# Optimization experiments

Measured on AMD Instinct MI355X. Metric: run time of the kernel, lower is better.

Reference implementation:

```python
import jax, jax.numpy as jnp
import numpy as np

D_MODEL = 512
N_HEADS = 8
D_K = D_MODEL // N_HEADS
D_FF = 2048
EPS = 1e-5  # torch LayerNorm default


def _layer_norm(x, g, b):
    mu = jnp.mean(x, axis=-1, keepdims=True)
    var = jnp.mean(jnp.square(x - mu), axis=-1, keepdims=True)
    return (x - mu) * jax.lax.rsqrt(var + EPS) * g + b


def setup_inputs() -> dict:
    key = jax.random.key(0)
    ks = jax.random.split(key, 16)
    s_in = 1.0 / np.sqrt(D_MODEL)
    s_ff = 1.0 / np.sqrt(D_FF)
    # Linear weights stored as [in, out] (transpose of torch convention)
    return {
        "x": jax.random.normal(ks[0], (2, 2048, D_MODEL), jnp.float32),
        "wq_w": jax.random.uniform(ks[1], (D_MODEL, D_MODEL), jnp.float32, -s_in, s_in),
        "wq_b": jax.random.uniform(ks[2], (D_MODEL,), jnp.float32, -s_in, s_in),
        "wk_w": jax.random.uniform(ks[3], (D_MODEL, D_MODEL), jnp.float32, -s_in, s_in),
        "wk_b": jax.random.uniform(ks[4], (D_MODEL,), jnp.float32, -s_in, s_in),
        "wv_w": jax.random.uniform(ks[5], (D_MODEL, D_MODEL), jnp.float32, -s_in, s_in),
        "wv_b": jax.random.uniform(ks[6], (D_MODEL,), jnp.float32, -s_in, s_in),
        "wo_w": jax.random.uniform(ks[7], (D_MODEL, D_MODEL), jnp.float32, -s_in, s_in),
        "wo_b": jax.random.uniform(ks[8], (D_MODEL,), jnp.float32, -s_in, s_in),
        "ln1_g": jnp.ones((D_MODEL,), jnp.float32),
        "ln1_b": jnp.zeros((D_MODEL,), jnp.float32),
        "fc1_w": jax.random.uniform(ks[9], (D_MODEL, D_FF), jnp.float32, -s_in, s_in),
        "fc1_b": jax.random.uniform(ks[10], (D_FF,), jnp.float32, -s_in, s_in),
        "fc2_w": jax.random.uniform(ks[11], (D_FF, D_MODEL), jnp.float32, -s_ff, s_ff),
        "fc2_b": jax.random.uniform(ks[12], (D_MODEL,), jnp.float32, -s_ff, s_ff),
        "ln2_g": jnp.ones((D_MODEL,), jnp.float32),
        "ln2_b": jnp.zeros((D_MODEL,), jnp.float32),
    }


def reference(x, wq_w, wq_b, wk_w, wk_b, wv_w, wv_b, wo_w, wo_b,
              ln1_g, ln1_b, fc1_w, fc1_b, fc2_w, fc2_b, ln2_g, ln2_b):
    B, T, _ = x.shape
    # --- multi-head self-attention (mask=None; dropout in eval mode = identity) ---
    q = (x @ wq_w + wq_b).reshape(B, T, N_HEADS, D_K).transpose(0, 2, 1, 3)  # [B,H,T,d_k]
    k = (x @ wk_w + wk_b).reshape(B, T, N_HEADS, D_K).transpose(0, 2, 1, 3)
    v = (x @ wv_w + wv_b).reshape(B, T, N_HEADS, D_K).transpose(0, 2, 1, 3)
    scores = jnp.einsum("bhqd,bhkd->bhqk", q, k) / np.sqrt(D_K).astype(np.float32)
    attn = jax.nn.softmax(scores, axis=-1)  # [B,H,T,T]
    ctx = jnp.einsum("bhqk,bhkd->bhqd", attn, v)
    ctx = ctx.transpose(0, 2, 1, 3).reshape(B, T, D_MODEL)
    attn_out = ctx @ wo_w + wo_b
    # --- residual + LN1 ---
    h = _layer_norm(x + attn_out, ln1_g, ln1_b)
    # --- FFN (relu) + residual + LN2 ---
    ffn = jax.nn.relu(h @ fc1_w + fc1_b) @ fc2_w + fc2_b
    out = _layer_norm(h + ffn, ln2_g, ln2_b)
    return out, attn
```

## Files before the change

### kernel.cpp

```cpp
#include <hip/hip_runtime.h>
#include <hip/hip_bf16.h>

typedef __hip_bfloat16 bf16;
typedef __attribute__((ext_vector_type(8))) short short8v;
typedef __attribute__((ext_vector_type(4))) float f32x4;

#define B_   2
#define T_   2048
#define D_   512
#define H_   8
#define DK_  64
#define DFF_ 2048
#define M_   (B_*T_)

static __device__ __forceinline__ float b2f(bf16 v) { return __bfloat162float(v); }
static __device__ __forceinline__ bf16  f2b(float v){ return __float2bfloat16(v); }

static __device__ __forceinline__ float ldin(const void* p, size_t i, bool bf) {
    return bf ? __bfloat162float(((const bf16*)p)[i]) : ((const float*)p)[i];
}
static __device__ __forceinline__ void stout(void* p, size_t i, float v, bool bf) {
    if (bf) ((bf16*)p)[i] = __float2bfloat16(v);
    else    ((float*)p)[i] = v;
}
static __device__ __forceinline__ short hi_of(float v) {
    bf16 h = f2b(v);
    return *(const short*)&h;
}
static __device__ __forceinline__ short lo_of(float v) {
    bf16 h = f2b(v);
    bf16 l = f2b(v - b2f(h));
    return *(const short*)&l;
}

__global__ void detect_dtype(const unsigned int* __restrict__ x, int* __restrict__ flag)
{
    __shared__ int cnt;
    if (threadIdx.x == 0) cnt = 0;
    __syncthreads();
    int local = 0;
    for (int i = threadIdx.x; i < 1024; i += 256) {
        unsigned int lo = x[i] & 0xFFFFu;
        float v = __uint_as_float(lo << 16);
        float a = fabsf(v);
        if (a > 1e-3f && a < 16.f) local++;
    }
    atomicAdd(&cnt, local);
    __syncthreads();
    if (threadIdx.x == 0) *flag = (cnt > 512) ? 1 : 0;
}

__global__ __launch_bounds__(256)
void split_x(const void* __restrict__ X, bf16* __restrict__ xh,
             bf16* __restrict__ xl, const int* __restrict__ flag)
{
    const bool bf = (*flag != 0);
    const size_t i = ((size_t)blockIdx.x * 256 + threadIdx.x) * 8;
    if (bf) {
        *(short8v*)(xh + i) = *(const short8v*)((const bf16*)X + i);
    } else {
        const float* Xf = (const float*)X + i;
        const float4 f0 = *(const float4*)(Xf);
        const float4 f1 = *(const float4*)(Xf + 4);
        const float vals[8] = {f0.x, f0.y, f0.z, f0.w, f1.x, f1.y, f1.z, f1.w};
        short8v hi, lo;
        #pragma unroll
        for (int j = 0; j < 8; ++j) {
            short th = hi_of(vals[j]);
            short tl = lo_of(vals[j]);
            hi[j] = th;
            lo[j] = tl;
        }
        *(short8v*)(xh + i) = hi;
        *(short8v*)(xl + i) = lo;
    }
}

__global__ __launch_bounds__(256)
void transpose_w(const void* __restrict__ W, bf16* __restrict__ oh,
                 bf16* __restrict__ ol, const int* __restrict__ flag,
                 int K, int N, float scale)
{
    const bool bf = (*flag != 0);
    __shared__ float tile[32][33];
    const int n0 = blockIdx.x * 32;
    const int k0 = blockIdx.y * 32;
    const int c  = threadIdx.x & 31;
    const int r8 = threadIdx.x >> 5;

    #pragma unroll
    for (int i = 0; i < 4; ++i) {
        int r = r8 + i * 8;
        tile[r][c] = ldin(W, (size_t)(k0 + r) * N + n0 + c, bf) * scale;
    }
    __syncthreads();
    #pragma unroll
    for (int i = 0; i < 4; ++i) {
        int r = r8 + i * 8;
        float v = tile[c][r];
        bf16 h = f2b(v);
        oh[(size_t)(n0 + r) * K + k0 + c] = h;
        if (!bf) ol[(size_t)(n0 + r) * K + k0 + c] = f2b(v - b2f(h));
    }
}

template<int BN, int NA, int RELU, int OBF>
__global__ __launch_bounds__(256)
void gemm_mfma(const bf16* __restrict__ Ahg, const bf16* __restrict__ Alg,
               const bf16* __restrict__ BTh, const bf16* __restrict__ BTl,
               const void* __restrict__ bias, const int* __restrict__ flag,
               void* __restrict__ C, bf16* __restrict__ Cl,
               int M, int N, int K, float bscale)
{
    constexpr int BM = 128;
    constexpr int FM = 4;
    constexpr int FN = BN / 32;
    const bool bfw   = (*flag != 0);
    const bool useAl = !(NA == 1 && bfw);
    const bool useBl = !bfw;

    __shared__ short As[2][BM][40];
    __shared__ short Bs[2][BN][40];

    const int tid  = threadIdx.x;
    const int lane = tid & 63;
    const int wave = tid >> 6;
    const int wm   = wave >> 1;
    const int wn   = wave & 1;
    const int rowBase = blockIdx.y * BM;
    const int colBase = blockIdx.x * BN;

    const int fr = lane & 15;
    const int kb = (lane >> 4) * 8;

    const int arow = tid >> 1;
    const int acol = (tid & 1) * 16;
    const int brow = (BN == 128) ? (tid >> 1) : (tid >> 2);
    const int bcol = (BN == 128) ? ((tid & 1) * 16) : ((tid & 3) * 8);

    const bf16* aHs = Ahg + (size_t)(rowBase + arow) * K + acol;
    const bf16* aLs = Alg + (size_t)(rowBase + arow) * K + acol;
    const bf16* bHs = BTh + (size_t)(colBase + brow) * K + bcol;
    const bf16* bLs = BTl + (size_t)(colBase + brow) * K + bcol;

    f32x4 acc[FM][FN] = {};

    for (int k0 = 0; k0 < K; k0 += 32) {
        __syncthreads();
        *(short8v*)&As[0][arow][acol]     = *(const short8v*)(aHs + k0);
        *(short8v*)&As[0][arow][acol + 8] = *(const short8v*)(aHs + k0 + 8);
        if (useAl) {
            *(short8v*)&As[1][arow][acol]     = *(const short8v*)(aLs + k0);
            *(short8v*)&As[1][arow][acol + 8] = *(const short8v*)(aLs + k0 + 8);
        }
        if (BN == 128) {
            *(short8v*)&Bs[0][brow][bcol]     = *(const short8v*)(bHs + k0);
            *(short8v*)&Bs[0][brow][bcol + 8] = *(const short8v*)(bHs + k0 + 8);
            if (useBl) {
                *(short8v*)&Bs[1][brow][bcol]     = *(const short8v*)(bLs + k0);
                *(short8v*)&Bs[1][brow][bcol + 8] = *(const short8v*)(bLs + k0 + 8);
            }
        } else {
            *(short8v*)&Bs[0][brow][bcol] = *(const short8v*)(bHs + k0);
            if (useBl)
                *(short8v*)&Bs[1][brow][bcol] = *(const short8v*)(bLs + k0);
        }
        __syncthreads();

        short8v aH[FM], aL[FM], bH[FN], bL[FN];
        #pragma unroll
        for (int f = 0; f < FM; ++f)
            aH[f] = *(const short8v*)&As[0][wm * 64 + f * 16 + fr][kb];
        if (useAl) {
            #pragma unroll
            for (int f = 0; f < FM; ++f)
                aL[f] = *(const short8v*)&As[1][wm * 64 + f * 16 + fr][kb];
        }
        #pragma unroll
        for (int f = 0; f < FN; ++f)
            bH[f] = *(const short8v*)&Bs[0][wn * (BN/2) + f * 16 + fr][kb];
        if (useBl) {
            #pragma unroll
            for (int f = 0; f < FN; ++f)
                bL[f] = *(const short8v*)&Bs[1][wn * (BN/2) + f * 16 + fr][kb];
        }

        #pragma unroll
        for (int i = 0; i < FM; ++i)
            #pragma unroll
            for (int j = 0; j < FN; ++j) {
                acc[i][j] = __builtin_amdgcn_mfma_f32_16x16x32_bf16(aH[i], bH[j], acc[i][j], 0, 0, 0);
                if (useAl)
                    acc[i][j] = __builtin_amdgcn_mfma_f32_16x16x32_bf16(aL[i], bH[j], acc[i][j], 0, 0, 0);
                if (useBl)
                    acc[i][j] = __builtin_amdgcn_mfma_f32_16x16x32_bf16(aH[i], bL[j], acc[i][j], 0, 0, 0);
            }
    }

    const int rq = (lane >> 4) * 4;
    #pragma unroll
    for (int j = 0; j < FN; ++j) {
        const int col = colBase + wn * (BN/2) + j * 16 + fr;
        const float bv = ldin(bias, col, bfw) * bscale;
        #pragma unroll
        for (int i = 0; i < FM; ++i) {
            #pragma unroll
            for (int q = 0; q < 4; ++q) {
                float v = acc[i][j][q] + bv;
                if (RELU) v = fmaxf(v, 0.f);
                const int row = rowBase + wm * 64 + i * 16 + rq + q;
                if (OBF == 0) {
                    ((float*)C)[(size_t)row * N + col] = v;
                } else if (OBF == 1) {
                    ((bf16*)C)[(size_t)row * N + col] = f2b(v);
                } else if (OBF == 2) {
                    size_t idx = (size_t)row * N + col;
                    bf16 h = f2b(v);
                    ((bf16*)C)[idx] = h;
                    Cl[idx] = f2b(v - b2f(h));
                } else {
                    ((bf16*)C)[(size_t)col * M + row] = f2b(v);
                }
            }
        }
    }
}

__global__ __launch_bounds__(256)
void attn_mfma(const bf16* __restrict__ Qb, const bf16* __restrict__ Kb,
               const bf16* __restrict__ VTb, void* __restrict__ dout,
               const int* __restrict__ flag,
               bf16* __restrict__ ctxh, bf16* __restrict__ ctxl)
{
    const bool bf = (*flag != 0);
    const int tid  = threadIdx.x;
    const int lane = tid & 63;
    const int wave = tid >> 6;
    const int wm = wave >> 1, wn = wave & 1;
    const int q0 = blockIdx.x * 64;
    const int h  = blockIdx.y;
    const int b  = blockIdx.z;
    const size_t OFFOUT = (size_t)M_ * D_;

    __shared__ short Qs[64][72];
    __shared__ short Ks[64][72];
    __shared__ short Vs[64][72];
    __shared__ short Ps[64][72];
    __shared__ float Lp[2][64];
    __shared__ float invl_s[64];

    const int fr = lane & 15;
    const int kb = (lane >> 4) * 8;

    #pragma unroll
    for (int l = 0; l < 2; ++l) {
        int idx = tid + l * 256;
        int r = idx >> 3, c8 = (idx & 7) * 8;
        *(short8v*)&Qs[r][c8] =
            *(const short8v*)(Qb + (size_t)(b*T_ + q0 + r) * D_ + h*DK_ + c8);
    }

    float lsum[2][4] = {};

    for (int kt = 0; kt < T_/64; ++kt) {
        __syncthreads();
        #pragma unroll
        for (int l = 0; l < 2; ++l) {
            int idx = tid + l * 256;
            int r = idx >> 3, c8 = (idx & 7) * 8;
            *(short8v*)&Ks[r][c8] =
                *(const short8v*)(Kb + (size_t)(b*T_ + kt*64 + r) * D_ + h*DK_ + c8);
        }
        __syncthreads();

        short8v aF[2][2], bF[2][2];
        #pragma unroll
        for (int i = 0; i < 2; ++i)
            #pragma unroll
            for (int k2 = 0; k2 < 2; ++k2)
                aF[i][k2] = *(const short8v*)&Qs[wm*32 + i*16 + fr][kb + k2*32];
        #pragma unroll
        for (int j = 0; j < 2; ++j)
            #pragma unroll
            for (int k2 = 0; k2 < 2; ++k2)
                bF[j][k2] = *(const short8v*)&Ks[wn*32 + j*16 + fr][kb + k2*32];

        #pragma unroll
        for (int i = 0; i < 2; ++i)
            #pragma unroll
            for (int j = 0; j < 2; ++j) {
                f32x4 s = {};
                s = __builtin_amdgcn_mfma_f32_16x16x32_bf16(aF[i][0], bF[j][0], s, 0, 0, 0);
                s = __builtin_amdgcn_mfma_f32_16x16x32_bf16(aF[i][1], bF[j][1], s, 0, 0, 0);
                #pragma unroll
                for (int q = 0; q < 4; ++q)
                    lsum[i][q] += __expf(fminf(s[q], 60.f));
            }
    }

    #pragma unroll
    for (int i = 0; i < 2; ++i)
        #pragma unroll
        for (int q = 0; q < 4; ++q) {
            float v = lsum[i][q];
            #pragma unroll
            for (int o = 8; o; o >>= 1) v += __shfl_xor(v, o, 16);
            lsum[i][q] = v;
        }
    if (fr == 0) {
        #pragma unroll
        for (int i = 0; i < 2; ++i)
            #pragma unroll
            for (int q = 0; q < 4; ++q)
                Lp[wn][wm*32 + i*16 + (lane>>4)*4 + q] = lsum[i][q];
    }
    __syncthreads();
    if (tid < 64) invl_s[tid] = 1.f / (Lp[0][tid] + Lp[1][tid]);
    __syncthreads();

    float il[2][4];
    #pragma unroll
    for (int i = 0; i < 2; ++i)
        #pragma unroll
        for (int q = 0; q < 4; ++q)
            il[i][q] = invl_s[wm*32 + i*16 + (lane>>4)*4 + q];

    f32x4 cacc[2][2] = {};

    for (int kt = 0; kt < T_/64; ++kt) {
        __syncthreads();
        #pragma unroll
        for (int l = 0; l < 2; ++l) {
            int idx = tid + l * 256;
            int r = idx >> 3, c8 = (idx & 7) * 8;
            *(short8v*)&Ks[r][c8] =
                *(const short8v*)(Kb + (size_t)(b*T_ + kt*64 + r) * D_ + h*DK_ + c8);
            *(short8v*)&Vs[r][c8] =
                *(const short8v*)(VTb + (size_t)(h*DK_ + r) * M_ + b*T_ + kt*64 + c8);
        }
        __syncthreads();

        short8v aF[2][2], bF[2][2];
        #pragma unroll
        for (int i = 0; i < 2; ++i)
            #pragma unroll
            for (int k2 = 0; k2 < 2; ++k2)
                aF[i][k2] = *(const short8v*)&Qs[wm*32 + i*16 + fr][kb + k2*32];
        #pragma unroll
        for (int j = 0; j < 2; ++j)
            #pragma unroll
            for (int k2 = 0; k2 < 2; ++k2)
                bF[j][k2] = *(const short8v*)&Ks[wn*32 + j*16 + fr][kb + k2*32];

        f32x4 sacc[2][2];
        #pragma unroll
        for (int i = 0; i < 2; ++i)
            #pragma unroll
            for (int j = 0; j < 2; ++j) {
                f32x4 s = {};
                s = __builtin_amdgcn_mfma_f32_16x16x32_bf16(aF[i][0], bF[j][0], s, 0, 0, 0);
                s = __builtin_amdgcn_mfma_f32_16x16x32_bf16(aF[i][1], bF[j][1], s, 0, 0, 0);
                sacc[i][j] = s;
            }

        #pragma unroll
        for (int i = 0; i < 2; ++i)
            #pragma unroll
            for (int j = 0; j < 2; ++j) {
                #pragma unroll
                for (int q = 0; q < 4; ++q) {
                    const int qq = wm*32 + i*16 + (lane>>4)*4 + q;
                    const int kk = wn*32 + j*16 + fr;
                    float p = __expf(fminf(sacc[i][j][q], 60.f)) * il[i][q];
                    bf16 pb = f2b(p);
                    Ps[qq][kk] = *(const short*)&pb;
                    size_t go = OFFOUT + ((size_t)((b*H_+h)*T_ + q0 + qq))*T_ + kt*64 + kk;
                    if (bf) ((bf16*)dout)[go] = pb;
                    else    ((float*)dout)[go] = p;
                }
            }
        __syncthreads();

        short8v pF[2][2], vF[2][2];
        #pragma unroll
        for (int i = 0; i < 2; ++i)
            #pragma unroll
            for (int k2 = 0; k2 < 2; ++k2)
                pF[i][k2] = *(const short8v*)&Ps[wm*32 + i*16 + fr][kb + k2*32];
        #pragma unroll
        for (int j = 0; j < 2; ++j)
            #pragma unroll
            for (int k2 = 0; k2 < 2; ++k2)
                vF[j][k2] = *(const short8v*)&Vs[wn*32 + j*16 + fr][kb + k2*32];

        #pragma unroll
        for (int i = 0; i < 2; ++i)
            #pragma unroll
            for (int j = 0; j < 2; ++j) {
                cacc[i][j] = __builtin_amdgcn_mfma_f32_16x16x32_bf16(pF[i][0], vF[j][0], cacc[i][j], 0, 0, 0);
                cacc[i][j] = __builtin_amdgcn_mfma_f32_16x16x32_bf16(pF[i][1], vF[j][1], cacc[i][j], 0, 0, 0);
            }
    }

    #pragma unroll
    for (int i = 0; i < 2; ++i)
        #pragma unroll
        for (int j = 0; j < 2; ++j)
            #pragma unroll
            for (int q = 0; q < 4; ++q) {
                const int qq = wm*32 + i*16 + (lane>>4)*4 + q;
                size_t idx = (size_t)(b*T_ + q0 + qq)*D_ + h*DK_ + wn*32 + j*16 + fr;
                float v = cacc[i][j][q];
                bf16 hh = f2b(v);
                ctxh[idx] = hh;
                ctxl[idx] = f2b(v - b2f(hh));
            }
}

__global__ __launch_bounds__(256)
void ln1_kernel(const void* X, const float* __restrict__ A,
                const void* g, const void* be,
                const int* __restrict__ flag, float* __restrict__ out,
                bf16* __restrict__ hh, bf16* __restrict__ hl)
{
    const bool bf = (*flag != 0);
    const int row = blockIdx.x;
    const int tid = threadIdx.x;
    const size_t base = (size_t)row * D_;

    float v0 = ldin(X, base + tid, bf)       + A[base + tid];
    float v1 = ldin(X, base + 256 + tid, bf) + A[base + 256 + tid];
    float s  = v0 + v1;
    float sq = v0*v0 + v1*v1;
    #pragma unroll
    for (int o = 32; o; o >>= 1) { s += __shfl_xor(s, o, 64); sq += __shfl_xor(sq, o, 64); }

    __shared__ float rs[4], rq[4];
    if ((tid & 63) == 0) { rs[tid >> 6] = s; rq[tid >> 6] = sq; }
    __syncthreads();
    s  = rs[0] + rs[1] + rs[2] + rs[3];
    sq = rq[0] + rq[1] + rq[2] + rq[3];

    float mu   = s * (1.f / D_);
    float var  = sq * (1.f / D_) - mu * mu;
    float rstd = rsqrtf(var + 1e-5f);
    float y0 = (v0 - mu) * rstd * ldin(g, tid, bf)       + ldin(be, tid, bf);
    float y1 = (v1 - mu) * rstd * ldin(g, 256 + tid, bf) + ldin(be, 256 + tid, bf);
    out[base + tid]       = y0;
    out[base + 256 + tid] = y1;
    bf16 h0 = f2b(y0); hh[base + tid] = h0;       hl[base + tid]       = f2b(y0 - b2f(h0));
    bf16 h1 = f2b(y1); hh[base + 256 + tid] = h1; hl[base + 256 + tid] = f2b(y1 - b2f(h1));
}

__global__ __launch_bounds__(256)
void ln2_kernel(const float* __restrict__ Hf, const float* __restrict__ F,
                const void* g, const void* be,
                const int* __restrict__ flag, void* out)
{
    const bool bf = (*flag != 0);
    const int row = blockIdx.x;
    const int tid = threadIdx.x;
    const size_t base = (size_t)row * D_;

    float v0 = Hf[base + tid]       + F[base + tid];
    float v1 = Hf[base + 256 + tid] + F[base + 256 + tid];
    float s  = v0 + v1;
    float sq = v0*v0 + v1*v1;
    #pragma unroll
    for (int o = 32; o; o >>= 1) { s += __shfl_xor(s, o, 64); sq += __shfl_xor(sq, o, 64); }

    __shared__ float rs[4], rq[4];
    if ((tid & 63) == 0) { rs[tid >> 6] = s; rq[tid >> 6] = sq; }
    __syncthreads();
    s  = rs[0] + rs[1] + rs[2] + rs[3];
    sq = rq[0] + rq[1] + rq[2] + rq[3];

    float mu   = s * (1.f / D_);
    float var  = sq * (1.f / D_) - mu * mu;
    float rstd = rsqrtf(var + 1e-5f);
    stout(out, base + tid,       (v0 - mu) * rstd * ldin(g, tid, bf)       + ldin(be, tid, bf),       bf);
    stout(out, base + 256 + tid, (v1 - mu) * rstd * ldin(g, 256 + tid, bf) + ldin(be, 256 + tid, bf), bf);
}

extern "C" void kernel_launch(void* const* d_in, const int* in_sizes, int n_in,
                              void* d_out, int out_size, void* d_ws, size_t ws_size,
                              hipStream_t stream)
{
    const void* x     = d_in[0];
    const void* wq_w  = d_in[1];
    const void* wq_b  = d_in[2];
    const void* wk_w  = d_in[3];
    const void* wk_b  = d_in[4];
    const void* wv_w  = d_in[5];
    const void* wv_b  = d_in[6];
    const void* wo_w  = d_in[7];
    const void* wo_b  = d_in[8];
    const void* ln1_g = d_in[9];
    const void* ln1_b = d_in[10];
    const void* fc1_w = d_in[11];
    const void* fc1_b = d_in[12];
    const void* fc2_w = d_in[13];
    const void* fc2_b = d_in[14];
    const void* ln2_g = d_in[15];
    const void* ln2_b = d_in[16];

    char* W = (char*)d_ws;
    const size_t MB = 1u << 20;
    bf16*  xh    = (bf16*)(W + 0*MB);
    bf16*  xl    = (bf16*)(W + 4*MB);
    bf16*  Qb    = (bf16*)(W + 8*MB);
    bf16*  Kb    = (bf16*)(W + 12*MB);
    bf16*  VTb   = (bf16*)(W + 16*MB);
    bf16*  ctxh  = (bf16*)(W + 20*MB);
    bf16*  ctxl  = (bf16*)(W + 24*MB);
    bf16*  ffn1h = (bf16*)(W + 0*MB);
    bf16*  ffn1l = (bf16*)(W + 16*MB);
    float* ao    = (float*)(W + 32*MB);
    float* ffn2  = (float*)(W + 32*MB);
    float* h     = (float*)(W + 40*MB);
    bf16*  hh    = (bf16*)(W + 48*MB);
    bf16*  hl    = (bf16*)(W + 52*MB);
    bf16*  tw    = (bf16*)(W + 56*MB);
    const size_t SW = (size_t)D_ * D_;
    const size_t SF = (size_t)D_ * DFF_;
    bf16* wqTh = tw;                 bf16* wqTl = wqTh + SW;
    bf16* wkTh = wqTl + SW;          bf16* wkTl = wkTh + SW;
    bf16* wvTh = wkTl + SW;          bf16* wvTl = wvTh + SW;
    bf16* woTh = wvTl + SW;          bf16* woTl = woTh + SW;
    bf16* f1Th = woTl + SW;          bf16* f1Tl = f1Th + SF;
    bf16* f2Th = f1Tl + SF;          bf16* f2Tl = f2Th + SF;
    int*  flag = (int*)(f2Tl + SF);

    dim3 blk(256);

    detect_dtype<<<1, 256, 0, stream>>>((const unsigned int*)x, flag);

    transpose_w<<<dim3(D_/32,   D_/32),   blk, 0, stream>>>(wq_w,  wqTh, wqTl, flag, D_,   D_,   0.125f);
    transpose_w<<<dim3(D_/32,   D_/32),   blk, 0, stream>>>(wk_w,  wkTh, wkTl, flag, D_,   D_,   1.f);
    transpose_w<<<dim3(D_/32,   D_/32),   blk, 0, stream>>>(wv_w,  wvTh, wvTl, flag, D_,   D_,   1.f);
    transpose_w<<<dim3(D_/32,   D_/32),   blk, 0, stream>>>(wo_w,  woTh, woTl, flag, D_,   D_,   1.f);
    transpose_w<<<dim3(DFF_/32, D_/32),   blk, 0, stream>>>(fc1_w, f1Th, f1Tl, flag, D_,   DFF_, 1.f);
    transpose_w<<<dim3(D_/32,   DFF_/32), blk, 0, stream>>>(fc2_w, f2Th, f2Tl, flag, DFF_, D_,   1.f);

    split_x<<<(M_*D_)/(256*8), blk, 0, stream>>>(x, xh, xl, flag);

    gemm_mfma<64,1,0,1><<<dim3(D_/64,  M_/128), blk, 0, stream>>>(xh, xl, wqTh, wqTl, wq_b, flag, Qb,  nullptr, M_, D_, D_, 0.125f);
    gemm_mfma<64,1,0,1><<<dim3(D_/64,  M_/128), blk, 0, stream>>>(xh, xl, wkTh, wkTl, wk_b, flag, Kb,  nullptr, M_, D_, D_, 1.f);
    gemm_mfma<64,1,0,3><<<dim3(D_/64,  M_/128), blk, 0, stream>>>(xh, xl, wvTh, wvTl, wv_b, flag, VTb, nullptr, M_, D_, D_, 1.f);

    attn_mfma<<<dim3(T_/64, H_, B_), blk, 0, stream>>>(Qb, Kb, VTb, d_out, flag, ctxh, ctxl);

    gemm_mfma<64,0,0,0><<<dim3(D_/64,  M_/128), blk, 0, stream>>>(ctxh, ctxl, woTh, woTl, wo_b, flag, ao, nullptr, M_, D_, D_, 1.f);

    ln1_kernel<<<M_, 256, 0, stream>>>(x, ao, ln1_g, ln1_b, flag, h, hh, hl);

    gemm_mfma<128,0,1,2><<<dim3(DFF_/128, M_/128), blk, 0, stream>>>(hh, hl, f1Th, f1Tl, fc1_b, flag, ffn1h, ffn1l, M_, DFF_, D_, 1.f);
    gemm_mfma<64,0,0,0><<<dim3(D_/64,   M_/128), blk, 0, stream>>>(ffn1h, ffn1l, f2Th, f2Tl, fc2_b, flag, ffn2, nullptr, M_, D_, DFF_, 1.f);

    ln2_kernel<<<M_, 256, 0, stream>>>(h, ffn2, ln2_g, ln2_b, flag, d_out);
}
```

Measured before the change: 686.1 us.

## Fuse weight prep and QKV GEMMs, shrink GEMM tiles, drop fp32 LN1 output

The six weight-transpose launches become one prep_weights kernel, and the three Q/K/V projections become one gemm_qkv launch over a concatenated 1536-wide weight. Every GEMM moves from a 128-row tile to a 64x64 tile, which gives more blocks for the small matrices. LN1 no longer writes a separate fp32 copy of h; LN2 rebuilds it from the bf16 hi/lo split. The aims are less launch overhead, better occupancy, and less memory traffic, at the cost of less reuse per tile and a small precision change in the residual.

```diff
diff --git a/kernel.cpp b/kernel.cpp
--- a/kernel.cpp
+++ b/kernel.cpp
@@ -77,14 +77,30 @@
 }
 
 __global__ __launch_bounds__(256)
-void transpose_w(const void* __restrict__ W, bf16* __restrict__ oh,
-                 bf16* __restrict__ ol, const int* __restrict__ flag,
-                 int K, int N, float scale)
+void prep_weights(const void* __restrict__ wq, const void* __restrict__ wk,
+                  const void* __restrict__ wv, const void* __restrict__ wo,
+                  const void* __restrict__ f1, const void* __restrict__ f2,
+                  bf16* __restrict__ qkvTh, bf16* __restrict__ qkvTl,
+                  bf16* __restrict__ woTh,  bf16* __restrict__ woTl,
+                  bf16* __restrict__ f1Th,  bf16* __restrict__ f1Tl,
+                  bf16* __restrict__ f2Th,  bf16* __restrict__ f2Tl,
+                  const int* __restrict__ flag)
 {
     const bool bf = (*flag != 0);
+    int bid = blockIdx.x;
+    const void* W; bf16 *oh, *ol; int K, N; float scale = 1.f;
+    if (bid < 256)       { W = wq; oh = qkvTh;          ol = qkvTl;          K = 512;  N = 512;  scale = 0.125f; }
+    else if (bid < 512)  { W = wk; oh = qkvTh + 262144; ol = qkvTl + 262144; K = 512;  N = 512;  bid -= 256; }
+    else if (bid < 768)  { W = wv; oh = qkvTh + 524288; ol = qkvTl + 524288; K = 512;  N = 512;  bid -= 512; }
+    else if (bid < 1024) { W = wo; oh = woTh;           ol = woTl;           K = 512;  N = 512;  bid -= 768; }
+    else if (bid < 2048) { W = f1; oh = f1Th;           ol = f1Tl;           K = 512;  N = 2048; bid -= 1024; }
+    else                 { W = f2; oh = f2Th;           ol = f2Tl;           K = 2048; N = 512;  bid -= 2048; }
+
+    const int ntn = N / 32;
+    const int n0 = (bid % ntn) * 32;
+    const int k0 = (bid / ntn) * 32;
+
     __shared__ float tile[32][33];
-    const int n0 = blockIdx.x * 32;
-    const int k0 = blockIdx.y * 32;
     const int c  = threadIdx.x & 31;
     const int r8 = threadIdx.x >> 5;
 
@@ -104,94 +120,162 @@
     }
 }
 
-template<int BN, int NA, int RELU, int OBF>
+__global__ __launch_bounds__(256)
+void gemm_qkv(const bf16* __restrict__ Ahg, const bf16* __restrict__ Alg,
+              const bf16* __restrict__ BTh, const bf16* __restrict__ BTl,
+              const void* __restrict__ qbias, const void* __restrict__ kbias,
+              const void* __restrict__ vbias, const int* __restrict__ flag,
+              bf16* __restrict__ Qb, bf16* __restrict__ Kb, bf16* __restrict__ VTb)
+{
+    const int  K     = D_;
+    const bool bfw   = (*flag != 0);
+    const bool useAl = !bfw;
+    const bool useBl = !bfw;
+
+    __shared__ short As[2][64][40];
+    __shared__ short Bs[2][64][40];
+
+    const int tid  = threadIdx.x;
+    const int lane = tid & 63;
+    const int wave = tid >> 6;
+    const int wm   = wave >> 1;
+    const int wn   = wave & 1;
+    const int rowBase = blockIdx.y * 64;
+    const int colBase = blockIdx.x * 64;
+
+    const int fr = lane & 15;
+    const int kb = (lane >> 4) * 8;
+    const int srow = tid >> 2;
+    const int skc  = (tid & 3) * 8;
+
+    const bf16* aHs = Ahg + (size_t)(rowBase + srow) * K + skc;
+    const bf16* aLs = Alg + (size_t)(rowBase + srow) * K + skc;
+    const bf16* bHs = BTh + (size_t)(colBase + srow) * K + skc;
+    const bf16* bLs = BTl + (size_t)(colBase + srow) * K + skc;
+
+    f32x4 acc[2][2] = {};
+
+    for (int k0 = 0; k0 < K; k0 += 32) {
+        __syncthreads();
+        *(short8v*)&As[0][srow][skc] = *(const short8v*)(aHs + k0);
+        if (useAl) *(short8v*)&As[1][srow][skc] = *(const short8v*)(aLs + k0);
+        *(short8v*)&Bs[0][srow][skc] = *(const short8v*)(bHs + k0);
+        if (useBl) *(short8v*)&Bs[1][srow][skc] = *(const short8v*)(bLs + k0);
+        __syncthreads();
+
+        short8v aH[2], aL[2], bH[2], bL[2];
+        #pragma unroll
+        for (int f = 0; f < 2; ++f) {
+            aH[f] = *(const short8v*)&As[0][wm * 32 + f * 16 + fr][kb];
+            bH[f] = *(const short8v*)&Bs[0][wn * 32 + f * 16 + fr][kb];
+        }
+        if (useAl) {
+            #pragma unroll
+            for (int f = 0; f < 2; ++f)
+                aL[f] = *(const short8v*)&As[1][wm * 32 + f * 16 + fr][kb];
+        }
+        if (useBl) {
+            #pragma unroll
+            for (int f = 0; f < 2; ++f)
+                bL[f] = *(const short8v*)&Bs[1][wn * 32 + f * 16 + fr][kb];
+        }
+
+        #pragma unroll
+        for (int i = 0; i < 2; ++i)
+            #pragma unroll
+            for (int j = 0; j < 2; ++j) {
+                acc[i][j] = __builtin_amdgcn_mfma_f32_16x16x32_bf16(aH[i], bH[j], acc[i][j], 0, 0, 0);
+                if (useAl)
+                    acc[i][j] = __builtin_amdgcn_mfma_f32_16x16x32_bf16(aL[i], bH[j], acc[i][j], 0, 0, 0);
+                if (useBl)
+                    acc[i][j] = __builtin_amdgcn_mfma_f32_16x16x32_bf16(aH[i], bL[j], acc[i][j], 0, 0, 0);
+            }
+    }
+
+    const int region = colBase >> 9;
+    const void* bp = (region == 0) ? qbias : (region == 1) ? kbias : vbias;
+    const float bs = (region == 0) ? 0.125f : 1.f;
+    const int rq = (lane >> 4) * 4;
+    #pragma unroll
+    for (int j = 0; j < 2; ++j) {
+        const int col = colBase + wn * 32 + j * 16 + fr;
+        const int lc  = col - (region << 9);
+        const float bv = ldin(bp, lc, bfw) * bs;
+        #pragma unroll
+        for (int i = 0; i < 2; ++i) {
+            #pragma unroll
+            for (int q = 0; q < 4; ++q) {
+                float v = acc[i][j][q] + bv;
+                const int row = rowBase + wm * 32 + i * 16 + rq + q;
+                if (region == 0)      Qb[(size_t)row * D_ + lc] = f2b(v);
+                else if (region == 1) Kb[(size_t)row * D_ + lc] = f2b(v);
+                else                  VTb[(size_t)lc * M_ + row] = f2b(v);
+            }
+        }
+    }
+}
+
+template<int RELU, int OBF>
 __global__ __launch_bounds__(256)
 void gemm_mfma(const bf16* __restrict__ Ahg, const bf16* __restrict__ Alg,
                const bf16* __restrict__ BTh, const bf16* __restrict__ BTl,
                const void* __restrict__ bias, const int* __restrict__ flag,
                void* __restrict__ C, bf16* __restrict__ Cl,
-               int M, int N, int K, float bscale)
-{
-    constexpr int BM = 128;
-    constexpr int FM = 4;
-    constexpr int FN = BN / 32;
+               int M, int N, int K)
+{
     const bool bfw   = (*flag != 0);
-    const bool useAl = !(NA == 1 && bfw);
     const bool useBl = !bfw;
 
-    __shared__ short As[2][BM][40];
-    __shared__ short Bs[2][BN][40];
+    __shared__ short As[2][64][40];
+    __shared__ short Bs[2][64][40];
 
     const int tid  = threadIdx.x;
     const int lane = tid & 63;
     const int wave = tid >> 6;
     const int wm   = wave >> 1;
     const int wn   = wave & 1;
-    const int rowBase = blockIdx.y * BM;
-    const int colBase = blockIdx.x * BN;
+    const int rowBase = blockIdx.y * 64;
+    const int colBase = blockIdx.x * 64;
 
     const int fr = lane & 15;
     const int kb = (lane >> 4) * 8;
-
-    const int arow = tid >> 1;
-    const int acol = (tid & 1) * 16;
-    const int brow = (BN == 128) ? (tid >> 1) : (tid >> 2);
-    const int bcol = (BN == 128) ? ((tid & 1) * 16) : ((tid & 3) * 8);
-
-    const bf16* aHs = Ahg + (size_t)(rowBase + arow) * K + acol;
-    const bf16* aLs = Alg + (size_t)(rowBase + arow) * K + acol;
-    const bf16* bHs = BTh + (size_t)(colBase + brow) * K + bcol;
-    const bf16* bLs = BTl + (size_t)(colBase + brow) * K + bcol;
-
-    f32x4 acc[FM][FN] = {};
+    const int srow = tid >> 2;
+    const int skc  = (tid & 3) * 8;
+
+    const bf16* aHs = Ahg + (size_t)(rowBase + srow) * K + skc;
+    const bf16* aLs = Alg + (size_t)(rowBase + srow) * K + skc;
+    const bf16* bHs = BTh + (size_t)(colBase + srow) * K + skc;
+    const bf16* bLs = BTl + (size_t)(colBase + srow) * K + skc;
+
+    f32x4 acc[2][2] = {};
 
     for (int k0 = 0; k0 < K; k0 += 32) {
         __syncthreads();
-        *(short8v*)&As[0][arow][acol]     = *(const short8v*)(aHs + k0);
-        *(short8v*)&As[0][arow][acol + 8] = *(const short8v*)(aHs + k0 + 8);
-        if (useAl) {
-            *(short8v*)&As[1][arow][acol]     = *(const short8v*)(aLs + k0);
-            *(short8v*)&As[1][arow][acol + 8] = *(const short8v*)(aLs + k0 + 8);
-        }
-        if (BN == 128) {
-            *(short8v*)&Bs[0][brow][bcol]     = *(const short8v*)(bHs + k0);
-            *(short8v*)&Bs[0][brow][bcol + 8] = *(const short8v*)(bHs + k0 + 8);
-            if (useBl) {
-                *(short8v*)&Bs[1][brow][bcol]     = *(const short8v*)(bLs + k0);
-                *(short8v*)&Bs[1][brow][bcol + 8] = *(const short8v*)(bLs + k0 + 8);
-            }
-        } else {
-            *(short8v*)&Bs[0][brow][bcol] = *(const short8v*)(bHs + k0);
-            if (useBl)
-                *(short8v*)&Bs[1][brow][bcol] = *(const short8v*)(bLs + k0);
-        }
-        __syncthreads();
-
-        short8v aH[FM], aL[FM], bH[FN], bL[FN];
-        #pragma unroll
-        for (int f = 0; f < FM; ++f)
-            aH[f] = *(const short8v*)&As[0][wm * 64 + f * 16 + fr][kb];
-        if (useAl) {
-            #pragma unroll
-            for (int f = 0; f < FM; ++f)
-                aL[f] = *(const short8v*)&As[1][wm * 64 + f * 16 + fr][kb];
-        }
-        #pragma unroll
-        for (int f = 0; f < FN; ++f)
-            bH[f] = *(const short8v*)&Bs[0][wn * (BN/2) + f * 16 + fr][kb];
+        *(short8v*)&As[0][srow][skc] = *(const short8v*)(aHs + k0);
+        *(short8v*)&As[1][srow][skc] = *(const short8v*)(aLs + k0);
+        *(short8v*)&Bs[0][srow][skc] = *(const short8v*)(bHs + k0);
+        if (useBl) *(short8v*)&Bs[1][srow][skc] = *(const short8v*)(bLs + k0);
+        __syncthreads();
+
+        short8v aH[2], aL[2], bH[2], bL[2];
+        #pragma unroll
+        for (int f = 0; f < 2; ++f) {
+            aH[f] = *(const short8v*)&As[0][wm * 32 + f * 16 + fr][kb];
+            aL[f] = *(const short8v*)&As[1][wm * 32 + f * 16 + fr][kb];
+            bH[f] = *(const short8v*)&Bs[0][wn * 32 + f * 16 + fr][kb];
+        }
         if (useBl) {
             #pragma unroll
-            for (int f = 0; f < FN; ++f)
-                bL[f] = *(const short8v*)&Bs[1][wn * (BN/2) + f * 16 + fr][kb];
-        }
-
-        #pragma unroll
-        for (int i = 0; i < FM; ++i)
-            #pragma unroll
-            for (int j = 0; j < FN; ++j) {
+            for (int f = 0; f < 2; ++f)
+                bL[f] = *(const short8v*)&Bs[1][wn * 32 + f * 16 + fr][kb];
+        }
+
+        #pragma unroll
+        for (int i = 0; i < 2; ++i)
+            #pragma unroll
+            for (int j = 0; j < 2; ++j) {
                 acc[i][j] = __builtin_amdgcn_mfma_f32_16x16x32_bf16(aH[i], bH[j], acc[i][j], 0, 0, 0);
-                if (useAl)
-                    acc[i][j] = __builtin_amdgcn_mfma_f32_16x16x32_bf16(aL[i], bH[j], acc[i][j], 0, 0, 0);
+                acc[i][j] = __builtin_amdgcn_mfma_f32_16x16x32_bf16(aL[i], bH[j], acc[i][j], 0, 0, 0);
                 if (useBl)
                     acc[i][j] = __builtin_amdgcn_mfma_f32_16x16x32_bf16(aH[i], bL[j], acc[i][j], 0, 0, 0);
             }
@@ -199,27 +283,23 @@
 
     const int rq = (lane >> 4) * 4;
     #pragma unroll
-    for (int j = 0; j < FN; ++j) {
-        const int col = colBase + wn * (BN/2) + j * 16 + fr;
-        const float bv = ldin(bias, col, bfw) * bscale;
-        #pragma unroll
-        for (int i = 0; i < FM; ++i) {
+    for (int j = 0; j < 2; ++j) {
+        const int col = colBase + wn * 32 + j * 16 + fr;
+        const float bv = ldin(bias, col, bfw);
+        #pragma unroll
+        for (int i = 0; i < 2; ++i) {
             #pragma unroll
             for (int q = 0; q < 4; ++q) {
                 float v = acc[i][j][q] + bv;
                 if (RELU) v = fmaxf(v, 0.f);
-                const int row = rowBase + wm * 64 + i * 16 + rq + q;
+                const int row = rowBase + wm * 32 + i * 16 + rq + q;
+                const size_t idx = (size_t)row * N + col;
                 if (OBF == 0) {
-                    ((float*)C)[(size_t)row * N + col] = v;
-                } else if (OBF == 1) {
-                    ((bf16*)C)[(size_t)row * N + col] = f2b(v);
-                } else if (OBF == 2) {
-                    size_t idx = (size_t)row * N + col;
+                    ((float*)C)[idx] = v;
+                } else {
                     bf16 h = f2b(v);
                     ((bf16*)C)[idx] = h;
                     Cl[idx] = f2b(v - b2f(h));
-                } else {
-                    ((bf16*)C)[(size_t)col * M + row] = f2b(v);
                 }
             }
         }
@@ -420,7 +500,7 @@
 __global__ __launch_bounds__(256)
 void ln1_kernel(const void* X, const float* __restrict__ A,
                 const void* g, const void* be,
-                const int* __restrict__ flag, float* __restrict__ out,
+                const int* __restrict__ flag,
                 bf16* __restrict__ hh, bf16* __restrict__ hl)
 {
     const bool bf = (*flag != 0);
@@ -446,14 +526,13 @@
     float rstd = rsqrtf(var + 1e-5f);
     float y0 = (v0 - mu) * rstd * ldin(g, tid, bf)       + ldin(be, tid, bf);
     float y1 = (v1 - mu) * rstd * ldin(g, 256 + tid, bf) + ldin(be, 256 + tid, bf);
-    out[base + tid]       = y0;
-    out[base + 256 + tid] = y1;
     bf16 h0 = f2b(y0); hh[base + tid] = h0;       hl[base + tid]       = f2b(y0 - b2f(h0));
     bf16 h1 = f2b(y1); hh[base + 256 + tid] = h1; hl[base + 256 + tid] = f2b(y1 - b2f(h1));
 }
 
 __global__ __launch_bounds__(256)
-void ln2_kernel(const float* __restrict__ Hf, const float* __restrict__ F,
+void ln2_kernel(const bf16* __restrict__ hh, const bf16* __restrict__ hl,
+                const float* __restrict__ F,
                 const void* g, const void* be,
                 const int* __restrict__ flag, void* out)
 {
@@ -462,8 +541,8 @@
     const int tid = threadIdx.x;
     const size_t base = (size_t)row * D_;
 
-    float v0 = Hf[base + tid]       + F[base + tid];
-    float v1 = Hf[base + 256 + tid] + F[base + 256 + tid];
+    float v0 = b2f(hh[base + tid])       + b2f(hl[base + tid])       + F[base + tid];
+    float v1 = b2f(hh[base + 256 + tid]) + b2f(hl[base + 256 + tid]) + F[base + 256 + tid];
     float s  = v0 + v1;
     float sq = v0*v0 + v1*v1;
     #pragma unroll
@@ -517,45 +596,46 @@
     bf16*  ffn1l = (bf16*)(W + 16*MB);
     float* ao    = (float*)(W + 32*MB);
     float* ffn2  = (float*)(W + 32*MB);
-    float* h     = (float*)(W + 40*MB);
-    bf16*  hh    = (bf16*)(W + 48*MB);
-    bf16*  hl    = (bf16*)(W + 52*MB);
-    bf16*  tw    = (bf16*)(W + 56*MB);
-    const size_t SW = (size_t)D_ * D_;
-    const size_t SF = (size_t)D_ * DFF_;
-    bf16* wqTh = tw;                 bf16* wqTl = wqTh + SW;
-    bf16* wkTh = wqTl + SW;          bf16* wkTl = wkTh + SW;
-    bf16* wvTh = wkTl + SW;          bf16* wvTl = wvTh + SW;
-    bf16* woTh = wvTl + SW;          bf16* woTl = woTh + SW;
-    bf16* f1Th = woTl + SW;          bf16* f1Tl = f1Th + SF;
-    bf16* f2Th = f1Tl + SF;          bf16* f2Tl = f2Th + SF;
-    int*  flag = (int*)(f2Tl + SF);
+    bf16*  hh    = (bf16*)(W + 40*MB);
+    bf16*  hl    = (bf16*)(W + 44*MB);
+    bf16*  tw    = (bf16*)(W + 48*MB);
+    const size_t SQKV = (size_t)1536 * 512;
+    const size_t SW   = (size_t)D_ * D_;
+    const size_t SF   = (size_t)D_ * DFF_;
+    bf16* qkvTh = tw;               bf16* qkvTl = qkvTh + SQKV;
+    bf16* woTh  = qkvTl + SQKV;     bf16* woTl  = woTh + SW;
+    bf16* f1Th  = woTl + SW;        bf16* f1Tl  = f1Th + SF;
+    bf16* f2Th  = f1Tl + SF;        bf16* f2Tl  = f2Th + SF;
+    int*  flag  = (int*)(f2Tl + SF);
 
     dim3 blk(256);
 
     detect_dtype<<<1, 256, 0, stream>>>((const unsigned int*)x, flag);
 
-    transpose_w<<<dim3(D_/32,   D_/32),   blk, 0, stream>>>(wq_w,  wqTh, wqTl, flag, D_,   D_,   0.125f);
-    transpose_w<<<dim3(D_/32,   D_/32),   blk, 0, stream>>>(wk_w,  wkTh, wkTl, flag, D_,   D_,   1.f);
-    transpose_w<<<dim3(D_/32,   D_/32),   blk, 0, stream>>>(wv_w,  wvTh, wvTl, flag, D_,   D_,   1.f);
-    transpose_w<<<dim3(D_/32,   D_/32),   blk, 0, stream>>>(wo_w,  woTh, woTl, flag, D_,   D_,   1.f);
-    transpose_w<<<dim3(DFF_/32, D_/32),   blk, 0, stream>>>(fc1_w, f1Th, f1Tl, flag, D_,   DFF_, 1.f);
-    transpose_w<<<dim3(D_/32,   DFF_/32), blk, 0, stream>>>(fc2_w, f2Th, f2Tl, flag, DFF_, D_,   1.f);
+    prep_weights<<<3072, blk, 0, stream>>>(wq_w, wk_w, wv_w, wo_w, fc1_w, fc2_w,
+                                           qkvTh, qkvTl, woTh, woTl,
+                                           f1Th, f1Tl, f2Th, f2Tl, flag);
 
     split_x<<<(M_*D_)/(256*8), blk, 0, stream>>>(x, xh, xl, flag);
 
-    gemm_mfma<64,1,0,1><<<dim3(D_/64,  M_/128), blk, 0, stream>>>(xh, xl, wqTh, wqTl, wq_b, flag, Qb,  nullptr, M_, D_, D_, 0.125f);
-    gemm_mfma<64,1,0,1><<<dim3(D_/64,  M_/128), blk, 0, stream>>>(xh, xl, wkTh, wkTl, wk_b, flag, Kb,  nullptr, M_, D_, D_, 1.f);
-    gemm_mfma<64,1,0,3><<<dim3(D_/64,  M_/128), blk, 0, stream>>>(xh, xl, wvTh, wvTl, wv_b, flag, VTb, nullptr, M_, D_, D_, 1.f);
+    gemm_qkv<<<dim3(1536/64, M_/64), blk, 0, stream>>>(xh, xl, qkvTh, qkvTl,
+                                                       wq_b, wk_b, wv_b, flag,
+                                                       Qb, Kb, VTb);
 
     attn_mfma<<<dim3(T_/64, H_, B_), blk, 0, stream>>>(Qb, Kb, VTb, d_out, flag, ctxh, ctxl);
 
-    gemm_mfma<64,0,0,0><<<dim3(D_/64,  M_/128), blk, 0, stream>>>(ctxh, ctxl, woTh, woTl, wo_b, flag, ao, nullptr, M_, D_, D_, 1.f);
-
-    ln1_kernel<<<M_, 256, 0, stream>>>(x, ao, ln1_g, ln1_b, flag, h, hh, hl);
-
-    gemm_mfma<128,0,1,2><<<dim3(DFF_/128, M_/128), blk, 0, stream>>>(hh, hl, f1Th, f1Tl, fc1_b, flag, ffn1h, ffn1l, M_, DFF_, D_, 1.f);
-    gemm_mfma<64,0,0,0><<<dim3(D_/64,   M_/128), blk, 0, stream>>>(ffn1h, ffn1l, f2Th, f2Tl, fc2_b, flag, ffn2, nullptr, M_, D_, DFF_, 1.f);
-
-    ln2_kernel<<<M_, 256, 0, stream>>>(h, ffn2, ln2_g, ln2_b, flag, d_out);
-}
+    gemm_mfma<0,0><<<dim3(D_/64, M_/64), blk, 0, stream>>>(ctxh, ctxl, woTh, woTl,
+                                                           wo_b, flag, ao, nullptr,
+                                                           M_, D_, D_);
+
+    ln1_kernel<<<M_, 256, 0, stream>>>(x, ao, ln1_g, ln1_b, flag, hh, hl);
+
+    gemm_mfma<1,2><<<dim3(DFF_/64, M_/64), blk, 0, stream>>>(hh, hl, f1Th, f1Tl,
+                                                             fc1_b, flag, ffn1h, ffn1l,
+                                                             M_, DFF_, D_);
+    gemm_mfma<0,0><<<dim3(D_/64, M_/64), blk, 0, stream>>>(ffn1h, ffn1l, f2Th, f2Tl,
+                                                           fc2_b, flag, ffn2, nullptr,
+                                                           M_, D_, DFF_);
+
+    ln2_kernel<<<M_, 256, 0, stream>>>(hh, hl, ffn2, ln2_g, ln2_b, flag, d_out);
+}
```

After: 607.9 us. -11.4%, faster.
